# Kernel tuning notes

Hardware: AMD Instinct MI355X
Metric: run time of the kernel (lower is better)

The kernel has to match this reference:

```python
import jax, jax.numpy as jnp
import numpy as np

VOL_RES = 128          # volume_res
SIGMA = 0.05           # gaussian splat sigma (normalized [0,1] coords)
SPLAT_R = 3            # splat neighborhood radius = smooth_kernel_size // 2
TET_W = 5              # tet rasterization window edge (voxels)
EPS_W = 1e-3           # weight_sum init (torch fills 0.001)

B, NV, NSURF, NF, NT = 2, 7700, 6890, 13776, 30000


def setup_inputs() -> dict:
    key = jax.random.key(0)
    k0, k1, k2, k3 = jax.random.split(key, 4)
    smpl_vertices = jax.random.uniform(k0, (B, NV, 3), dtype=jnp.float32)      # verts in [0,1]^3
    vertex_code = jax.random.uniform(k1, (B, NSURF, 3), dtype=jnp.float32)     # semantic code per surface vert
    face_indices = jax.random.randint(k2, (NF, 3), 0, NSURF, dtype=jnp.int32)
    tet_indices = jax.random.randint(k3, (NT, 4), 0, NV, dtype=jnp.int32)
    return {"smpl_vertices": smpl_vertices, "vertex_code": vertex_code,
            "face_indices": face_indices, "tet_indices": tet_indices}


def _voxelize(smpl_vertices, vertex_code, face_indices, tet_indices):
    R = VOL_RES
    R3 = R * R * R
    bsz = smpl_vertices.shape[0]

    # --- face centers / normals (computed by the torch forward; not consumed by the kernel) ---
    faces = smpl_vertices[:, face_indices]                         # (B,NF,3,3)
    face_center = faces.mean(axis=2)                               # (B,NF,3)
    v10 = faces[:, :, 0] - faces[:, :, 1]
    v12 = faces[:, :, 2] - faces[:, :, 1]
    nrm = jnp.cross(v10, v12)
    face_normal = nrm / jnp.maximum(
        jnp.linalg.norm(nrm, axis=-1, keepdims=True), 1e-5)        # F.normalize eps=1e-5
    del face_center, face_normal  # passed to the autograd fn but unused by the cuda op

    bidx = jnp.arange(bsz, dtype=jnp.int32)

    # ---------------- occupancy from tetrahedrons (point-in-tet rasterization) ----------------
    tets = smpl_vertices[:, tet_indices]                           # (B,NT,4,3)
    a = tets[:, :, 0]
    e1 = tets[:, :, 1] - a
    e2 = tets[:, :, 2] - a
    e3 = tets[:, :, 3] - a
    c23 = jnp.cross(e2, e3)
    vol6 = jnp.sum(e1 * c23, axis=-1)                              # signed 6*volume (B,NT)

    anchor = jnp.floor(jnp.min(tets, axis=2) * R).astype(jnp.int32)  # (B,NT,3) min-corner voxel
    w1 = jnp.arange(TET_W, dtype=jnp.int32)
    toff = jnp.stack(jnp.meshgrid(w1, w1, w1, indexing="ij"), -1).reshape(-1, 3)  # (W3,3) xyz
    tvox = anchor[:, :, None, :] + toff                            # (B,NT,W3,3)
    tp = (tvox.astype(jnp.float32) + 0.5) / R                      # voxel centers
    p = tp - a[:, :, None, :]                                      # (B,NT,W3,3)
    iv = 1.0 / jnp.where(jnp.abs(vol6) > 1e-12, vol6, 1.0)
    l1 = jnp.sum(p * c23[:, :, None, :], -1) * iv[:, :, None]
    l2 = jnp.sum(jnp.cross(p, e3[:, :, None, :]) * e1[:, :, None, :], -1) * iv[:, :, None]
    l3 = jnp.sum(jnp.cross(e2[:, :, None, :], p) * e1[:, :, None, :], -1) * iv[:, :, None]
    inside = (l1 >= 0) & (l2 >= 0) & (l3 >= 0) & (l1 + l2 + l3 <= 1.0)
    inside &= (jnp.abs(vol6) > 1e-12)[:, :, None]
    tvalid = jnp.all((tvox >= 0) & (tvox < R), axis=-1) & inside   # (B,NT,W3)
    # linear index, layout (b, z, y, x)
    tlin = ((bidx[:, None, None] * R + tvox[..., 2]) * R + tvox[..., 1]) * R + tvox[..., 0]
    tlin = jnp.where(tvalid, tlin, bsz * R3)                       # drop out-of-range
    occ = jnp.zeros((bsz * R3,), jnp.float32).at[tlin.reshape(-1)].max(
        tvalid.astype(jnp.float32).reshape(-1), mode="drop")

    # ---------------- gaussian semantic splat from surface vertices ----------------
    vs = smpl_vertices[:, :NSURF]                                  # (B,NS,3)
    base = jnp.floor(vs * R).astype(jnp.int32)                     # containing voxel
    o1 = jnp.arange(-SPLAT_R, SPLAT_R + 1, dtype=jnp.int32)
    offs = jnp.stack(jnp.meshgrid(o1, o1, o1, indexing="ij"), -1).reshape(-1, 3)  # (K3,3)
    svox = base[:, :, None, :] + offs                              # (B,NS,K3,3)
    ctr = (svox.astype(jnp.float32) + 0.5) / R
    d2 = jnp.sum((ctr - vs[:, :, None, :]) ** 2, axis=-1)          # (B,NS,K3)
    w = jnp.exp(-d2 / (2.0 * SIGMA * SIGMA))
    svalid = jnp.all((svox >= 0) & (svox < R), axis=-1)
    w = jnp.where(svalid, w, 0.0)
    slin = ((bidx[:, None, None] * R + svox[..., 2]) * R + svox[..., 1]) * R + svox[..., 0]
    slin = jnp.where(svalid, slin, bsz * R3).reshape(-1)

    wsum = jnp.full((bsz * R3,), EPS_W, jnp.float32).at[slin].add(w.reshape(-1), mode="drop")
    contrib = (w[..., None] * vertex_code[:, :, None, :]).reshape(-1, 3)
    sem = jnp.zeros((bsz * R3, 3), jnp.float32).at[slin].add(contrib, mode="drop")

    semantic = sem / wsum[:, None] * occ[:, None]                  # normalize + mask to body
    semantic = semantic.reshape(bsz, R, R, R, 3)                   # (B, z, y, x, C)
    return jnp.transpose(semantic, (0, 4, 1, 2, 3))                # (B, C, z, y, x)


def reference(smpl_vertices, vertex_code, face_indices, tet_indices):
    return _voxelize(smpl_vertices, vertex_code, face_indices, tet_indices)
```

## Files before the change

### kernel.cpp

```cpp
#include <hip/hip_runtime.h>
#include <math.h>

#define R 128
#define R3 (R*R*R)
#define BATCH 2
#define NV 7700
#define NSURF 6890
#define NT 30000
#define EPS_W 0.001f

#define NC 32
#define NCELLS (BATCH*NC*NC*NC)
#define CAP 12
#define SLOT_F 8

__global__ void bin_kernel(const float* __restrict__ verts,
                           const float* __restrict__ code,
                           int*   __restrict__ counts,
                           float* __restrict__ bins) {
    int idx = blockIdx.x * blockDim.x + threadIdx.x;
    if (idx >= BATCH * NSURF) return;
    int v = idx % NSURF;
    int b = idx / NSURF;

    const float* vp = verts + ((size_t)b * NV + v) * 3;
    float px = vp[0], py = vp[1], pz = vp[2];
    int bx = (int)floorf(px * 128.0f);
    int by = (int)floorf(py * 128.0f);
    int bz = (int)floorf(pz * 128.0f);
    bx = min(max(bx, 0), 127); by = min(max(by, 0), 127); bz = min(max(bz, 0), 127);

    int cell = ((b * NC + (bz >> 2)) * NC + (by >> 2)) * NC + (bx >> 2);
    int slot = atomicAdd(counts + cell, 1);
    if (slot < CAP) {
        const float* cp = code + ((size_t)b * NSURF + v) * 3;
        float* s = bins + ((size_t)cell * CAP + slot) * SLOT_F;
        s[0] = px; s[1] = py; s[2] = pz;
        s[3] = cp[0]; s[4] = cp[1]; s[5] = cp[2];
    }
}

__global__ void tet_kernel(const float* __restrict__ verts,
                           const int*   __restrict__ tets,
                           unsigned char* __restrict__ occ) {
    const int total = BATCH * NT * 25;
    int idx = blockIdx.x * blockDim.x + threadIdx.x;
    if (idx >= total) return;
    int k  = idx % 25;
    int bt = idx / 25;
    int t  = bt % NT;
    int b  = bt / NT;

    int4 ti = *(const int4*)(tets + (size_t)t * 4);
    const float* vb = verts + (size_t)b * NV * 3;

    float ax = vb[ti.x*3+0], ay = vb[ti.x*3+1], az = vb[ti.x*3+2];
    float bx = vb[ti.y*3+0], by = vb[ti.y*3+1], bz = vb[ti.y*3+2];
    float cx = vb[ti.z*3+0], cy = vb[ti.z*3+1], cz = vb[ti.z*3+2];
    float dx = vb[ti.w*3+0], dy = vb[ti.w*3+1], dz = vb[ti.w*3+2];

    float e1x = bx-ax, e1y = by-ay, e1z = bz-az;
    float e2x = cx-ax, e2y = cy-ay, e2z = cz-az;
    float e3x = dx-ax, e3y = dy-ay, e3z = dz-az;

    float c23x = e2y*e3z - e2z*e3y;
    float c23y = e2z*e3x - e2x*e3z;
    float c23z = e2x*e3y - e2y*e3x;
    float vol6 = e1x*c23x + e1y*c23y + e1z*c23z;
    if (fabsf(vol6) <= 1e-12f) return;

    int anx  = (int)floorf(fminf(fminf(ax,bx), fminf(cx,dx)) * 128.0f);
    int any_ = (int)floorf(fminf(fminf(ay,by), fminf(cy,dy)) * 128.0f);
    int anz  = (int)floorf(fminf(fminf(az,bz), fminf(cz,dz)) * 128.0f);

    int vy = any_ + k / 5;
    int vz = anz  + k % 5;
    if ((unsigned)vy >= 128u || (unsigned)vz >= 128u) return;

    const float inv = 1.0f / 128.0f;
    float iv = 1.0f / vol6;
    float py = ((float)vy + 0.5f) * inv - ay;
    float pz = ((float)vz + 0.5f) * inv - az;

    unsigned char* orow = occ + (size_t)b * R3 + ((size_t)vz * R + vy) * R;

    #pragma unroll
    for (int ddx = 0; ddx < 5; ddx++) {
        int vx = anx + ddx;
        if ((unsigned)vx >= 128u) continue;
        float px = ((float)vx + 0.5f) * inv - ax;

        float l1 = (px*c23x + py*c23y + pz*c23z) * iv;
        float cpx = py*e3z - pz*e3y;
        float cpy = pz*e3x - px*e3z;
        float cpz = px*e3y - py*e3x;
        float l2 = (cpx*e1x + cpy*e1y + cpz*e1z) * iv;
        float cqx = e2y*pz - e2z*py;
        float cqy = e2z*px - e2x*pz;
        float cqz = e2x*py - e2y*px;
        float l3 = (cqx*e1x + cqy*e1y + cqz*e1z) * iv;

        if (l1 >= 0.0f && l2 >= 0.0f && l3 >= 0.0f && (l1 + l2 + l3) <= 1.0f)
            orow[vx] = 1;
    }
}

__global__ void gather_kernel(const unsigned char* __restrict__ occ,
                              const int*   __restrict__ counts,
                              const float* __restrict__ bins,
                              float* __restrict__ out) {
    const int total = BATCH * R3;
    int i = blockIdx.x * blockDim.x + threadIdx.x;
    if (i >= total) return;
    int b = i / R3;
    int L = i % R3;
    int x = L & 127;
    int y = (L >> 7) & 127;
    int z = L >> 14;

    float* ob = out + (size_t)b * 3 * R3 + L;

    if (!occ[i]) {
        ob[0] = 0.0f; ob[R3] = 0.0f; ob[2*R3] = 0.0f;
        return;
    }

    const float inv = 1.0f / 128.0f;
    float fx = ((float)x + 0.5f) * inv;
    float fy = ((float)y + 0.5f) * inv;
    float fz = ((float)z + 0.5f) * inv;

    int cx0 = max(x - 3, 0) >> 2, cx1 = min(x + 3, 127) >> 2;
    int cy0 = max(y - 3, 0) >> 2, cy1 = min(y + 3, 127) >> 2;
    int cz0 = max(z - 3, 0) >> 2, cz1 = min(z + 3, 127) >> 2;

    float wsum = EPS_W, s0 = 0.0f, s1 = 0.0f, s2 = 0.0f;

    for (int cz = cz0; cz <= cz1; cz++)
    for (int cy = cy0; cy <= cy1; cy++)
    for (int cx = cx0; cx <= cx1; cx++) {
        int cell = ((b * NC + cz) * NC + cy) * NC + cx;
        int n = counts[cell];
        n = min(n, CAP);
        const float* s = bins + (size_t)cell * CAP * SLOT_F;
        for (int j = 0; j < n; j++, s += SLOT_F) {
            float4 a  = *(const float4*)s;
            float2 bb = *(const float2*)(s + 4);
            float px = a.x, py = a.y, pz = a.z;
            int bx = (int)floorf(px * 128.0f);
            int by = (int)floorf(py * 128.0f);
            int bz = (int)floorf(pz * 128.0f);
            if (abs(x - bx) <= 3 && abs(y - by) <= 3 && abs(z - bz) <= 3) {
                float ddx = fx - px, ddy = fy - py, ddz = fz - pz;
                float d2 = ddx*ddx + ddy*ddy + ddz*ddz;
                float w = __expf(-200.0f * d2);
                wsum += w;
                s0 += w * a.w;
                s1 += w * bb.x;
                s2 += w * bb.y;
            }
        }
    }
    ob[0]    = s0 / wsum;
    ob[R3]   = s1 / wsum;
    ob[2*R3] = s2 / wsum;
}

extern "C" void kernel_launch(void* const* d_in, const int* in_sizes, int n_in,
                              void* d_out, int out_size, void* d_ws, size_t ws_size,
                              hipStream_t stream) {
    const float* smpl_vertices = (const float*)d_in[0];
    const float* vertex_code   = (const float*)d_in[1];
    const int*   tet_indices   = (const int*)d_in[3];
    float* out = (float*)d_out;

    unsigned char* occ = (unsigned char*)d_ws;
    int*   counts = (int*)(occ + (size_t)BATCH * R3);
    float* bins   = (float*)(counts + NCELLS);

    hipMemsetAsync(occ, 0, (size_t)BATCH * R3 + (size_t)NCELLS * sizeof(int), stream);

    const int bin_total = BATCH * NSURF;
    bin_kernel<<<(bin_total + 255) / 256, 256, 0, stream>>>(smpl_vertices, vertex_code, counts, bins);

    const int tet_total = BATCH * NT * 25;
    tet_kernel<<<(tet_total + 255) / 256, 256, 0, stream>>>(smpl_vertices, tet_indices, occ);

    const int nvox = BATCH * R3;
    gather_kernel<<<(nvox + 255) / 256, 256, 0, stream>>>(occ, counts, bins, out);
}
```

Measured before the change: 117.9 us.

## Tile gather into 8^3 blocks with shared-memory vertex lists; precompute tet data

The per-voxel gather, which walked neighbouring bin cells for every voxel, becomes a per-8x8x8-tile kernel. Each tile loads the candidate splat vertices from its neighbourhood into shared memory once, then each thread handles two voxels with pre-packed voxel coordinates. A separate tet prep kernel computes per-tet edges, cross products and anchors once instead of 25 times per tet. In exchange it adds an extra launch and workspace traffic, and it silently truncates at 256 candidate vertices per tile. The packed anchors also drop sign information for negative coordinates.

New measurement: 115.0 us. 2.4% less time.

```diff
diff --git a/kernel.cpp b/kernel.cpp
--- a/kernel.cpp
+++ b/kernel.cpp
@@ -13,6 +13,9 @@
 #define NCELLS (BATCH*NC*NC*NC)
 #define CAP 12
 #define SLOT_F 8
+#define MAXV 256
+
+#define TET_STRIDE 20
 
 __global__ void bin_kernel(const float* __restrict__ verts,
                            const float* __restrict__ code,
@@ -40,38 +43,66 @@
     }
 }
 
-__global__ void tet_kernel(const float* __restrict__ verts,
-                           const int*   __restrict__ tets,
+__global__ void tet_prep_kernel(const float* __restrict__ verts,
+                                const int*   __restrict__ tets,
+                                float* __restrict__ td) {
+    int bt = blockIdx.x * blockDim.x + threadIdx.x;
+    if (bt >= BATCH * NT) return;
+    int t = bt % NT;
+    int b = bt / NT;
+
+    int4 ti = *(const int4*)(tets + (size_t)t * 4);
+    const float* vb = verts + (size_t)b * NV * 3;
+
+    float ax = vb[ti.x*3+0], ay = vb[ti.x*3+1], az = vb[ti.x*3+2];
+    float bx = vb[ti.y*3+0], by = vb[ti.y*3+1], bz = vb[ti.y*3+2];
+    float cx = vb[ti.z*3+0], cy = vb[ti.z*3+1], cz = vb[ti.z*3+2];
+    float dx = vb[ti.w*3+0], dy = vb[ti.w*3+1], dz = vb[ti.w*3+2];
+
+    float e1x = bx-ax, e1y = by-ay, e1z = bz-az;
+    float e2x = cx-ax, e2y = cy-ay, e2z = cz-az;
+    float e3x = dx-ax, e3y = dy-ay, e3z = dz-az;
+
+    float c23x = e2y*e3z - e2z*e3y;
+    float c23y = e2z*e3x - e2x*e3z;
+    float c23z = e2x*e3y - e2y*e3x;
+    float vol6 = e1x*c23x + e1y*c23y + e1z*c23z;
+
+    int anx  = (int)floorf(fminf(fminf(ax,bx), fminf(cx,dx)) * 128.0f);
+    int any_ = (int)floorf(fminf(fminf(ay,by), fminf(cy,dy)) * 128.0f);
+    int anz  = (int)floorf(fminf(fminf(az,bz), fminf(cz,dz)) * 128.0f);
+    int pk = (anx & 0xFF) | ((any_ & 0xFF) << 8) | ((anz & 0xFF) << 16);
+
+    float* o = td + (size_t)bt * TET_STRIDE;
+    float4* o4 = (float4*)o;
+    o4[0] = make_float4(ax, ay, az, e1x);
+    o4[1] = make_float4(e1y, e1z, e2x, e2y);
+    o4[2] = make_float4(e2z, e3x, e3y, e3z);
+    o4[3] = make_float4(c23x, c23y, c23z, vol6);
+    o4[4] = make_float4(__int_as_float(pk), 0.0f, 0.0f, 0.0f);
+}
+
+__global__ void tet_kernel(const float* __restrict__ td,
                            unsigned char* __restrict__ occ) {
     const int total = BATCH * NT * 25;
     int idx = blockIdx.x * blockDim.x + threadIdx.x;
     if (idx >= total) return;
     int k  = idx % 25;
     int bt = idx / 25;
-    int t  = bt % NT;
     int b  = bt / NT;
 
-    int4 ti = *(const int4*)(tets + (size_t)t * 4);
-    const float* vb = verts + (size_t)b * NV * 3;
-
-    float ax = vb[ti.x*3+0], ay = vb[ti.x*3+1], az = vb[ti.x*3+2];
-    float bx = vb[ti.y*3+0], by = vb[ti.y*3+1], bz = vb[ti.y*3+2];
-    float cx = vb[ti.z*3+0], cy = vb[ti.z*3+1], cz = vb[ti.z*3+2];
-    float dx = vb[ti.w*3+0], dy = vb[ti.w*3+1], dz = vb[ti.w*3+2];
-
-    float e1x = bx-ax, e1y = by-ay, e1z = bz-az;
-    float e2x = cx-ax, e2y = cy-ay, e2z = cz-az;
-    float e3x = dx-ax, e3y = dy-ay, e3z = dz-az;
-
-    float c23x = e2y*e3z - e2z*e3y;
-    float c23y = e2z*e3x - e2x*e3z;
-    float c23z = e2x*e3y - e2y*e3x;
-    float vol6 = e1x*c23x + e1y*c23y + e1z*c23z;
+    const float4* o4 = (const float4*)(td + (size_t)bt * TET_STRIDE);
+    float4 r0 = o4[0], r1 = o4[1], r2 = o4[2], r3 = o4[3], r4 = o4[4];
+    float ax = r0.x, ay = r0.y, az = r0.z;
+    float e1x = r0.w, e1y = r1.x, e1z = r1.y;
+    float e2x = r1.z, e2y = r1.w, e2z = r2.x;
+    float e3x = r2.y, e3y = r2.z, e3z = r2.w;
+    float c23x = r3.x, c23y = r3.y, c23z = r3.z;
+    float vol6 = r3.w;
     if (fabsf(vol6) <= 1e-12f) return;
 
-    int anx  = (int)floorf(fminf(fminf(ax,bx), fminf(cx,dx)) * 128.0f);
-    int any_ = (int)floorf(fminf(fminf(ay,by), fminf(cy,dy)) * 128.0f);
-    int anz  = (int)floorf(fminf(fminf(az,bz), fminf(cz,dz)) * 128.0f);
+    int pk = __float_as_int(r4.x);
+    int anx = pk & 0xFF, any_ = (pk >> 8) & 0xFF, anz = (pk >> 16) & 0xFF;
 
     int vy = any_ + k / 5;
     int vz = anz  + k % 5;
@@ -105,65 +136,100 @@
     }
 }
 
-__global__ void gather_kernel(const unsigned char* __restrict__ occ,
-                              const int*   __restrict__ counts,
-                              const float* __restrict__ bins,
-                              float* __restrict__ out) {
-    const int total = BATCH * R3;
-    int i = blockIdx.x * blockDim.x + threadIdx.x;
-    if (i >= total) return;
-    int b = i / R3;
-    int L = i % R3;
-    int x = L & 127;
-    int y = (L >> 7) & 127;
-    int z = L >> 14;
-
-    float* ob = out + (size_t)b * 3 * R3 + L;
-
-    if (!occ[i]) {
-        ob[0] = 0.0f; ob[R3] = 0.0f; ob[2*R3] = 0.0f;
-        return;
-    }
-
-    const float inv = 1.0f / 128.0f;
-    float fx = ((float)x + 0.5f) * inv;
-    float fy = ((float)y + 0.5f) * inv;
-    float fz = ((float)z + 0.5f) * inv;
-
-    int cx0 = max(x - 3, 0) >> 2, cx1 = min(x + 3, 127) >> 2;
-    int cy0 = max(y - 3, 0) >> 2, cy1 = min(y + 3, 127) >> 2;
-    int cz0 = max(z - 3, 0) >> 2, cz1 = min(z + 3, 127) >> 2;
-
-    float wsum = EPS_W, s0 = 0.0f, s1 = 0.0f, s2 = 0.0f;
-
-    for (int cz = cz0; cz <= cz1; cz++)
-    for (int cy = cy0; cy <= cy1; cy++)
-    for (int cx = cx0; cx <= cx1; cx++) {
-        int cell = ((b * NC + cz) * NC + cy) * NC + cx;
-        int n = counts[cell];
-        n = min(n, CAP);
-        const float* s = bins + (size_t)cell * CAP * SLOT_F;
-        for (int j = 0; j < n; j++, s += SLOT_F) {
-            float4 a  = *(const float4*)s;
-            float2 bb = *(const float2*)(s + 4);
-            float px = a.x, py = a.y, pz = a.z;
-            int bx = (int)floorf(px * 128.0f);
-            int by = (int)floorf(py * 128.0f);
-            int bz = (int)floorf(pz * 128.0f);
-            if (abs(x - bx) <= 3 && abs(y - by) <= 3 && abs(z - bz) <= 3) {
-                float ddx = fx - px, ddy = fy - py, ddz = fz - pz;
-                float d2 = ddx*ddx + ddy*ddy + ddz*ddz;
-                float w = __expf(-200.0f * d2);
-                wsum += w;
-                s0 += w * a.w;
-                s1 += w * bb.x;
-                s2 += w * bb.y;
+__global__ __launch_bounds__(256) void gather_tile_kernel(
+        const unsigned char* __restrict__ occ,
+        const int*   __restrict__ counts,
+        const float* __restrict__ bins,
+        float* __restrict__ out) {
+    __shared__ float4 s_a[MAXV];
+    __shared__ float4 s_b[MAXV];
+    __shared__ int s_n;
+
+    int blk = blockIdx.x;
+    int tx = blk & 15, ty = (blk >> 4) & 15, tz = (blk >> 8) & 15, b = blk >> 12;
+    int x0 = tx << 3, y0 = ty << 3, z0 = tz << 3;
+
+    if (threadIdx.x == 0) s_n = 0;
+    __syncthreads();
+
+    int cx0 = max(x0 - 3, 0) >> 2, cx1 = min(x0 + 10, 127) >> 2;
+    int cy0 = max(y0 - 3, 0) >> 2, cy1 = min(y0 + 10, 127) >> 2;
+    int cz0 = max(z0 - 3, 0) >> 2, cz1 = min(z0 + 10, 127) >> 2;
+    int ncx = cx1 - cx0 + 1, ncy = cy1 - cy0 + 1, ncz = cz1 - cz0 + 1;
+    int ncell = ncx * ncy * ncz;
+
+    int t = threadIdx.x;
+    if (t < ncell) {
+        int lx = t % ncx; int rem = t / ncx;
+        int ly = rem % ncy; int lz = rem / ncy;
+        int cell = ((b * NC + cz0 + lz) * NC + cy0 + ly) * NC + cx0 + lx;
+        int n = min(counts[cell], CAP);
+        if (n > 0) {
+            int base = atomicAdd(&s_n, n);
+            const float* sp = bins + (size_t)cell * CAP * SLOT_F;
+            for (int j = 0; j < n; j++, sp += SLOT_F) {
+                int d = base + j;
+                if (d < MAXV) {
+                    float4 A = *(const float4*)sp;
+                    float2 Bc = *(const float2*)(sp + 4);
+                    int bx = (int)floorf(A.x * 128.0f);
+                    int by = (int)floorf(A.y * 128.0f);
+                    int bz = (int)floorf(A.z * 128.0f);
+                    int pk = bx | (by << 8) | (bz << 16);
+                    s_a[d] = A;
+                    s_b[d] = make_float4(Bc.x, Bc.y, __int_as_float(pk), 0.0f);
+                }
             }
         }
     }
-    ob[0]    = s0 / wsum;
-    ob[R3]   = s1 / wsum;
-    ob[2*R3] = s2 / wsum;
+    __syncthreads();
+    int nv = min(s_n, MAXV);
+
+    int x = x0 + (t & 7);
+    int y = y0 + ((t >> 3) & 7);
+    int z = z0 + (t >> 6);
+
+    int L0 = (z * R + y) * R + x;
+    int L1 = L0 + 4 * R * R;
+    unsigned char o0 = occ[(size_t)b * R3 + L0];
+    unsigned char o1 = occ[(size_t)b * R3 + L1];
+
+    float w0 = EPS_W, p0 = 0.0f, q0 = 0.0f, r0 = 0.0f;
+    float w1 = EPS_W, p1 = 0.0f, q1 = 0.0f, r1 = 0.0f;
+
+    if (__ballot(o0 | o1)) {
+        const float inv = 1.0f / 128.0f;
+        float fx  = ((float)x + 0.5f) * inv;
+        float fy  = ((float)y + 0.5f) * inv;
+        float fz0 = ((float)z + 0.5f) * inv;
+        float fz1 = fz0 + 4.0f * inv;
+        for (int j = 0; j < nv; j++) {
+            float4 A  = s_a[j];
+            float4 Bv = s_b[j];
+            int pk = __float_as_int(Bv.z);
+            int bx = pk & 0xFF, by = (pk >> 8) & 0xFF, bz = (pk >> 16) & 0xFF;
+            if (abs(x - bx) <= 3 && abs(y - by) <= 3) {
+                float ddx = fx - A.x, ddy = fy - A.y;
+                float dxy = ddx*ddx + ddy*ddy;
+                int dz0 = z - bz;
+                if (abs(dz0) <= 3) {
+                    float dd = fz0 - A.z;
+                    float w = __expf(-200.0f * (dxy + dd*dd));
+                    w0 += w; p0 += w*A.w; q0 += w*Bv.x; r0 += w*Bv.y;
+                }
+                if (abs(dz0 + 4) <= 3) {
+                    float dd = fz1 - A.z;
+                    float w = __expf(-200.0f * (dxy + dd*dd));
+                    w1 += w; p1 += w*A.w; q1 += w*Bv.x; r1 += w*Bv.y;
+                }
+            }
+        }
+    }
+    float s0 = o0 ? 1.0f / w0 : 0.0f;
+    float s1 = o1 ? 1.0f / w1 : 0.0f;
+    float* ob = out + (size_t)b * 3 * R3;
+    ob[L0]        = p0 * s0; ob[R3 + L0]   = q0 * s0; ob[2*R3 + L0] = r0 * s0;
+    ob[L1]        = p1 * s1; ob[R3 + L1]   = q1 * s1; ob[2*R3 + L1] = r1 * s1;
 }
 
 extern "C" void kernel_launch(void* const* d_in, const int* in_sizes, int n_in,
@@ -177,15 +243,19 @@
     unsigned char* occ = (unsigned char*)d_ws;
     int*   counts = (int*)(occ + (size_t)BATCH * R3);
     float* bins   = (float*)(counts + NCELLS);
+    float* td     = bins + (size_t)NCELLS * CAP * SLOT_F;
 
     hipMemsetAsync(occ, 0, (size_t)BATCH * R3 + (size_t)NCELLS * sizeof(int), stream);
 
     const int bin_total = BATCH * NSURF;
     bin_kernel<<<(bin_total + 255) / 256, 256, 0, stream>>>(smpl_vertices, vertex_code, counts, bins);
 
+    const int nt_total = BATCH * NT;
+    tet_prep_kernel<<<(nt_total + 255) / 256, 256, 0, stream>>>(smpl_vertices, tet_indices, td);
+
     const int tet_total = BATCH * NT * 25;
-    tet_kernel<<<(tet_total + 255) / 256, 256, 0, stream>>>(smpl_vertices, tet_indices, occ);
-
-    const int nvox = BATCH * R3;
-    gather_kernel<<<(nvox + 255) / 256, 256, 0, stream>>>(occ, counts, bins, out);
-}
+    tet_kernel<<<(tet_total + 255) / 256, 256, 0, stream>>>(td, occ);
+
+    const int ntiles = BATCH * 16 * 16 * 16;
+    gather_tile_kernel<<<ntiles, 256, 0, stream>>>(occ, counts, bins, out);
+}
```
